# Kernel optimization log

Measured on AMD Instinct MI355X. Metric: run time of the kernel, lower is better.

Reference implementation:

```python
import jax, jax.numpy as jnp
import numpy as np

NUM_HEADS = 16

def setup_inputs() -> dict:
    key = jax.random.key(0)
    ks = jax.random.split(key, 7)
    B, S, D = 2, 2048, 1024
    X = jax.random.normal(ks[0], (B, S, D), dtype=jnp.float32)
    s = 1.0 / np.sqrt(D)
    Wq = jax.random.normal(ks[1], (D, D), dtype=jnp.float32) * s
    Wk = jax.random.normal(ks[2], (D, D), dtype=jnp.float32) * s
    Wv = jax.random.normal(ks[3], (D, D), dtype=jnp.float32) * s
    Wo = jax.random.normal(ks[4], (D, D), dtype=jnp.float32) * s
    bo = jnp.zeros((D,), dtype=jnp.float32)
    return {"X": X, "Wq": Wq, "Wk": Wk, "Wv": Wv, "Wo": Wo, "bo": bo}

def reference(X, Wq, Wk, Wv, Wo, bo):
    B, S, D = X.shape
    H = NUM_HEADS
    hd = D // H
    # project and split heads -> [B, H, S, hd]
    def split(t):
        return t.reshape(B, S, H, hd).transpose(0, 2, 1, 3)
    q = split(X @ Wq)
    k = split(X @ Wk)
    v = split(X @ Wv)
    scores = jnp.einsum('bhqd,bhkd->bhqk', q, k) / jnp.sqrt(jnp.float32(hd))
    causal = jnp.tril(jnp.ones((S, S), dtype=bool))
    scores = jnp.where(causal, scores, -jnp.inf)
    weights = jax.nn.softmax(scores, axis=-1)  # dropout p=0 -> identity
    ctx = jnp.einsum('bhqk,bhkd->bhqd', weights, v)
    ctx = ctx.transpose(0, 2, 1, 3).reshape(B, S, D)
    return ctx @ Wo + bo
```

## Files before the change

### kernel.cpp

```cpp
#include <hip/hip_runtime.h>


typedef __attribute__((ext_vector_type(8))) short short8;
typedef __attribute__((ext_vector_type(4))) float floatx4;

__device__ inline float bf2f(unsigned short u) {
  return __uint_as_float(((unsigned)u) << 16);
}
__device__ inline unsigned short f2bf(float f) {
  unsigned u = __float_as_uint(f);
  unsigned r = (u + 0x7fffu + ((u >> 16) & 1u)) >> 16;
  return (unsigned short)r;
}

__device__ __forceinline__ void gll16(const unsigned short* g, unsigned short* l) {
  __builtin_amdgcn_global_load_lds(
      (const __attribute__((address_space(1))) unsigned int*)(g),
      (__attribute__((address_space(3))) unsigned int*)(l),
      16, 0, 0);
}

constexpr int B_ = 2, S_ = 2048, D_ = 1024, H_ = 16, HD_ = 64;

__global__ __launch_bounds__(256) void convert_x(
    const float* __restrict__ x, unsigned short* __restrict__ xb)
{
  const size_t i = ((size_t)blockIdx.x * 256 + threadIdx.x) * 8;
  float4 a = *(const float4*)(x + i);
  float4 b = *(const float4*)(x + i + 4);
  short8 o;
  o[0] = (short)f2bf(a.x); o[1] = (short)f2bf(a.y);
  o[2] = (short)f2bf(a.z); o[3] = (short)f2bf(a.w);
  o[4] = (short)f2bf(b.x); o[5] = (short)f2bf(b.y);
  o[6] = (short)f2bf(b.z); o[7] = (short)f2bf(b.w);
  *(short8*)(xb + i) = o;
}

__global__ __launch_bounds__(256) void transpose_convert_w4(
    const float* __restrict__ w0, const float* __restrict__ w1,
    const float* __restrict__ w2, const float* __restrict__ w3,
    unsigned short* __restrict__ wt_base)
{
  const float* src;
  switch (blockIdx.z) {
    case 0: src = w0; break;
    case 1: src = w1; break;
    case 2: src = w2; break;
    default: src = w3; break;
  }
  unsigned short* dst = wt_base + (size_t)blockIdx.z * 1024 * 1024;
  __shared__ unsigned short t[32][33];
  const int bx = blockIdx.x * 32;
  const int by = blockIdx.y * 32;
  const int x = threadIdx.x;
  for (int yy = threadIdx.y; yy < 32; yy += 8)
    t[yy][x] = f2bf(src[(size_t)(by + yy) * 1024 + bx + x]);
  __syncthreads();
  for (int yy = threadIdx.y; yy < 32; yy += 8)
    dst[(size_t)(bx + yy) * 1024 + by + x] = t[x][yy];
}

__global__ __launch_bounds__(256) void transpose_v(
    const unsigned short* __restrict__ Vb, unsigned short* __restrict__ Vt)
{
  __shared__ unsigned short t[32][33];
  const int bh = blockIdx.z;
  const int b = bh >> 4, h = bh & 15;
  const int s0 = blockIdx.x * 32, d0 = blockIdx.y * 32;
  const int x = threadIdx.x;
  for (int yy = threadIdx.y; yy < 32; yy += 8)
    t[yy][x] = Vb[(size_t)(b * 2048 + s0 + yy) * 1024 + h * 64 + d0 + x];
  __syncthreads();
  for (int yy = threadIdx.y; yy < 32; yy += 8)
    Vt[((size_t)bh * 64 + d0 + yy) * 2048 + s0 + x] = t[x][yy];
}

struct GemmAcc { floatx4 a[4][4]; };

__device__ __forceinline__ void gemm256_core(
    const unsigned short* __restrict__ A,
    const unsigned short* __restrict__ Bt,
    int m0, int bn0, int K,
    unsigned short* sA, unsigned short* sB, GemmAcc& acc)
{
  const int tid = threadIdx.x, wave = tid >> 6, lane = tid & 63;
  const int g = lane >> 4, ml = lane & 15;
  const int wm = wave & 1, wn = wave >> 1;

  const unsigned short* ag0 = A + (size_t)(m0 + (tid >> 2)) * K + (tid & 3) * 8;
  const unsigned short* ag1 = ag0 + (size_t)64 * K;
  const unsigned short* bg0 = Bt + (size_t)(bn0 + (tid >> 2)) * K + (tid & 3) * 8;
  const unsigned short* bg1 = bg0 + (size_t)64 * K;
  unsigned short* sAw0 = sA + wave * 512;
  unsigned short* sAw1 = sA + 2048 + wave * 512;
  unsigned short* sBw0 = sB + wave * 512;
  unsigned short* sBw1 = sB + 2048 + wave * 512;

#pragma unroll
  for (int mt = 0; mt < 4; ++mt)
#pragma unroll
    for (int nt = 0; nt < 4; ++nt) acc.a[mt][nt] = (floatx4){0.f, 0.f, 0.f, 0.f};

  for (int k0 = 0; k0 < K; k0 += 32) {
    __syncthreads();
    gll16(ag0 + k0, sAw0);
    gll16(ag1 + k0, sAw1);
    gll16(bg0 + k0, sBw0);
    gll16(bg1 + k0, sBw1);
    __syncthreads();
    short8 af[4], bf[4];
#pragma unroll
    for (int mt = 0; mt < 4; ++mt)
      af[mt] = *(const short8*)(sA + (wm * 64 + mt * 16 + ml) * 32 + g * 8);
#pragma unroll
    for (int nt = 0; nt < 4; ++nt)
      bf[nt] = *(const short8*)(sB + (wn * 64 + nt * 16 + ml) * 32 + g * 8);
#pragma unroll
    for (int mt = 0; mt < 4; ++mt)
#pragma unroll
      for (int nt = 0; nt < 4; ++nt)
        acc.a[mt][nt] = __builtin_amdgcn_mfma_f32_16x16x32_bf16(
            af[mt], bf[nt], acc.a[mt][nt], 0, 0, 0);
  }
}

__global__ __launch_bounds__(256) void gemm256_qkv(
    const unsigned short* __restrict__ A,
    const unsigned short* __restrict__ Bt,
    unsigned short* __restrict__ Qo,
    unsigned short* __restrict__ Ko,
    unsigned short* __restrict__ Vo)
{
  __shared__ unsigned short sA[128 * 32];
  __shared__ unsigned short sB[128 * 32];
  const int m0 = blockIdx.y * 128;
  const int bn0 = blockIdx.x * 128;
  GemmAcc acc;
  gemm256_core(A, Bt, m0, bn0, 1024, sA, sB, acc);

  const int proj = blockIdx.x >> 3;
  unsigned short* out = (proj == 0) ? Qo : (proj == 1) ? Ko : Vo;
  const int col0 = (blockIdx.x & 7) * 128;
  const int tid = threadIdx.x, wave = tid >> 6, lane = tid & 63;
  const int g = lane >> 4, ml = lane & 15;
  const int wm = wave & 1, wn = wave >> 1;
#pragma unroll
  for (int mt = 0; mt < 4; ++mt) {
#pragma unroll
    for (int nt = 0; nt < 4; ++nt) {
      const int col = col0 + wn * 64 + nt * 16 + ml;
#pragma unroll
      for (int r = 0; r < 4; ++r) {
        const int row = m0 + wm * 64 + mt * 16 + g * 4 + r;
        out[(size_t)row * 1024 + col] = f2bf(acc.a[mt][nt][r]);
      }
    }
  }
}

__global__ __launch_bounds__(256) void gemm256_wo(
    const unsigned short* __restrict__ A,
    const unsigned short* __restrict__ Bt,
    const float* __restrict__ bias,
    float* __restrict__ C)
{
  __shared__ unsigned short sA[128 * 32];
  __shared__ unsigned short sB[128 * 32];
  const int m0 = blockIdx.y * 128;
  const int bn0 = blockIdx.x * 128;
  GemmAcc acc;
  gemm256_core(A, Bt, m0, bn0, 1024, sA, sB, acc);

  const int tid = threadIdx.x, wave = tid >> 6, lane = tid & 63;
  const int g = lane >> 4, ml = lane & 15;
  const int wm = wave & 1, wn = wave >> 1;
#pragma unroll
  for (int mt = 0; mt < 4; ++mt) {
#pragma unroll
    for (int nt = 0; nt < 4; ++nt) {
      const int col = bn0 + wn * 64 + nt * 16 + ml;
      const float badd = bias[col];
#pragma unroll
      for (int r = 0; r < 4; ++r) {
        const int row = m0 + wm * 64 + mt * 16 + g * 4 + r;
        C[(size_t)row * 1024 + col] = acc.a[mt][nt][r] + badd;
      }
    }
  }
}

constexpr int LDP = 72;

__device__ __forceinline__ void attn_tile(
    const short8* aq,
    const unsigned short* sK0, const unsigned short* sK1,
    const unsigned short* sV0, const unsigned short* sV1,
    unsigned short* pw, floatx4* acc, float* l,
    const bool diag, const int qrow0, const int kcol0,
    const int g, const int ml)
{
  floatx4 s[4];
#pragma unroll
  for (int nb = 0; nb < 4; ++nb) {
    s[nb] = (floatx4){0.f, 0.f, 0.f, 0.f};
    short8 bk0 = *(const short8*)(sK0 + (nb * 16 + ml) * 32 + g * 8);
    s[nb] = __builtin_amdgcn_mfma_f32_16x16x32_bf16(aq[0], bk0, s[nb], 0, 0, 0);
    short8 bk1 = *(const short8*)(sK1 + (nb * 16 + ml) * 32 + g * 8);
    s[nb] = __builtin_amdgcn_mfma_f32_16x16x32_bf16(aq[1], bk1, s[nb], 0, 0, 0);
  }
#pragma unroll
  for (int r = 0; r < 4; ++r) {
    const int qrow = qrow0 + g * 4 + r;
    float rowsum = 0.f;
#pragma unroll
    for (int nb = 0; nb < 4; ++nb) {
      float wv = __expf(fmaf(s[nb][r], 0.125f, -24.0f));
      if (diag && (kcol0 + nb * 16 + ml > qrow)) wv = 0.f;
      rowsum += wv;
      pw[(g * 4 + r) * LDP + nb * 16 + ml] = f2bf(wv);
    }
    l[r] += rowsum;
  }
#pragma unroll
  for (int st = 0; st < 2; ++st) {
    short8 ap = *(const short8*)(pw + ml * LDP + st * 32 + g * 8);
    const unsigned short* sv = st ? sV1 : sV0;
#pragma unroll
    for (int jd = 0; jd < 4; ++jd) {
      short8 bv = *(const short8*)(sv + (jd * 16 + ml) * 32 + g * 8);
      acc[jd] = __builtin_amdgcn_mfma_f32_16x16x32_bf16(ap, bv, acc[jd], 0, 0, 0);
    }
  }
}

__global__ __launch_bounds__(256) void attn_v2(
    const unsigned short* __restrict__ Q,
    const unsigned short* __restrict__ Kg,
    const unsigned short* __restrict__ Vt,
    unsigned short* __restrict__ CTX)
{
  __shared__ unsigned short sK0[64 * 32], sK1[64 * 32];
  __shared__ unsigned short sV0[64 * 32], sV1[64 * 32];
  __shared__ unsigned short sP[4 * 16 * LDP];

  const int bh = blockIdx.y;
  const int b = bh >> 4, h = bh & 15;
  const int p = blockIdx.x;
  const int qbA = p, qbB = 31 - p;
  const int qA0 = qbA * 64, qB0 = qbB * 64;
  const int tid = threadIdx.x, wave = tid >> 6, lane = tid & 63;
  const int g = lane >> 4, ml = lane & 15;

  const size_t headoff = (size_t)b * S_ * D_ + (size_t)h * HD_;
  const size_t vtoff   = (size_t)bh * HD_ * S_;

  short8 aqA[2], aqB[2];
  {
    const unsigned short* qp =
        Q + headoff + (size_t)(qA0 + wave * 16 + ml) * D_ + g * 8;
    aqA[0] = *(const short8*)qp;
    aqA[1] = *(const short8*)(qp + 32);
  }
  {
    const unsigned short* qp =
        Q + headoff + (size_t)(qB0 + wave * 16 + ml) * D_ + g * 8;
    aqB[0] = *(const short8*)qp;
    aqB[1] = *(const short8*)(qp + 32);
  }

  floatx4 accA[4], accB[4];
#pragma unroll
  for (int jd = 0; jd < 4; ++jd) {
    accA[jd] = (floatx4){0.f, 0.f, 0.f, 0.f};
    accB[jd] = (floatx4){0.f, 0.f, 0.f, 0.f};
  }
  float lA[4] = {0.f, 0.f, 0.f, 0.f};
  float lB[4] = {0.f, 0.f, 0.f, 0.f};

  const int srow = lane >> 2;
  const int schunk = (lane & 3) * 8;
  const unsigned short* kgb =
      Kg + headoff + (size_t)(wave * 16 + srow) * D_ + schunk;
  const unsigned short* vgb =
      Vt + vtoff + (size_t)(wave * 16 + srow) * S_ + schunk;
  unsigned short* sk0w = sK0 + wave * 16 * 32;
  unsigned short* sk1w = sK1 + wave * 16 * 32;
  unsigned short* sv0w = sV0 + wave * 16 * 32;
  unsigned short* sv1w = sV1 + wave * 16 * 32;
  unsigned short* pw = sP + wave * 16 * LDP;

  for (int kt = 0; kt <= qbB; ++kt) {
    __syncthreads();
    const size_t ko = (size_t)kt * 64 * D_;
    gll16(kgb + ko, sk0w);
    gll16(kgb + ko + 32, sk1w);
    gll16(vgb + kt * 64, sv0w);
    gll16(vgb + kt * 64 + 32, sv1w);
    __syncthreads();

    attn_tile(aqB, sK0, sK1, sV0, sV1, pw, accB, lB,
              kt == qbB, qB0 + wave * 16, kt * 64, g, ml);
    if (kt <= qbA)
      attn_tile(aqA, sK0, sK1, sV0, sV1, pw, accA, lA,
                kt == qbA, qA0 + wave * 16, kt * 64, g, ml);
  }

#pragma unroll
  for (int r = 0; r < 4; ++r) {
    float la = lA[r];
    la += __shfl_xor(la, 1); la += __shfl_xor(la, 2);
    la += __shfl_xor(la, 4); la += __shfl_xor(la, 8);
    lA[r] = 1.0f / la;
    float lb = lB[r];
    lb += __shfl_xor(lb, 1); lb += __shfl_xor(lb, 2);
    lb += __shfl_xor(lb, 4); lb += __shfl_xor(lb, 8);
    lB[r] = 1.0f / lb;
  }
#pragma unroll
  for (int r = 0; r < 4; ++r) {
    const int rowA = qA0 + wave * 16 + g * 4 + r;
    const int rowB = qB0 + wave * 16 + g * 4 + r;
#pragma unroll
    for (int jd = 0; jd < 4; ++jd) {
      CTX[headoff + (size_t)rowA * D_ + jd * 16 + ml] = f2bf(accA[jd][r] * lA[r]);
      CTX[headoff + (size_t)rowB * D_ + jd * 16 + ml] = f2bf(accB[jd][r] * lB[r]);
    }
  }
}

constexpr int LDK = 40;

__global__ __launch_bounds__(256) void gemm_f32_bf16(
    const float* __restrict__ A, const float* __restrict__ B,
    unsigned short* __restrict__ C, int M, int N, int K)
{
  __shared__ unsigned short sA[64 * LDK];
  __shared__ unsigned short sB[64 * LDK];
  const int tid = threadIdx.x, wave = tid >> 6, lane = tid & 63;
  const int n0 = blockIdx.x * 64, m0 = blockIdx.y * 64;
  const int a_row = tid >> 2, a_k = (tid & 3) * 8;
  const float* Ag = A + (size_t)(m0 + a_row) * K + a_k;
  unsigned short* sAw = sA + a_row * LDK + a_k;
  const int b_k = tid >> 3, b_n = (tid & 7) * 8;
  const float* Bg = B + (size_t)b_k * N + n0 + b_n;
  unsigned short* sBw = sB + b_n * LDK + b_k;
  const int q = lane >> 4, ml = lane & 15;
  const unsigned short* sAr = sA + (wave * 16 + ml) * LDK + q * 8;
  const unsigned short* sBr = sB + ml * LDK + q * 8;
  floatx4 acc[4];
#pragma unroll
  for (int j = 0; j < 4; ++j) acc[j] = (floatx4){0.f, 0.f, 0.f, 0.f};
  for (int k0 = 0; k0 < K; k0 += 32) {
    float4 av0 = *(const float4*)(Ag + k0);
    float4 av1 = *(const float4*)(Ag + k0 + 4);
    float4 bv0 = *(const float4*)(Bg + (size_t)k0 * N);
    float4 bv1 = *(const float4*)(Bg + (size_t)k0 * N + 4);
    short8 av;
    av[0] = (short)f2bf(av0.x); av[1] = (short)f2bf(av0.y);
    av[2] = (short)f2bf(av0.z); av[3] = (short)f2bf(av0.w);
    av[4] = (short)f2bf(av1.x); av[5] = (short)f2bf(av1.y);
    av[6] = (short)f2bf(av1.z); av[7] = (short)f2bf(av1.w);
    __syncthreads();
    *(short8*)sAw = av;
    sBw[0 * LDK] = f2bf(bv0.x); sBw[1 * LDK] = f2bf(bv0.y);
    sBw[2 * LDK] = f2bf(bv0.z); sBw[3 * LDK] = f2bf(bv0.w);
    sBw[4 * LDK] = f2bf(bv1.x); sBw[5 * LDK] = f2bf(bv1.y);
    sBw[6 * LDK] = f2bf(bv1.z); sBw[7 * LDK] = f2bf(bv1.w);
    __syncthreads();
    short8 af = *(const short8*)sAr;
#pragma unroll
    for (int j = 0; j < 4; ++j) {
      short8 bf = *(const short8*)(sBr + j * 16 * LDK);
      acc[j] = __builtin_amdgcn_mfma_f32_16x16x32_bf16(af, bf, acc[j], 0, 0, 0);
    }
  }
#pragma unroll
  for (int j = 0; j < 4; ++j) {
    const int col = n0 + j * 16 + ml;
#pragma unroll
    for (int r = 0; r < 4; ++r) {
      const int row = m0 + wave * 16 + q * 4 + r;
      C[(size_t)row * N + col] = f2bf(acc[j][r]);
    }
  }
}

__global__ __launch_bounds__(256) void gemm_bf16_f32(
    const unsigned short* __restrict__ A, const float* __restrict__ B,
    const float* __restrict__ bias, float* __restrict__ C, int M, int N, int K)
{
  __shared__ unsigned short sA[64 * LDK];
  __shared__ unsigned short sB[64 * LDK];
  const int tid = threadIdx.x, wave = tid >> 6, lane = tid & 63;
  const int n0 = blockIdx.x * 64, m0 = blockIdx.y * 64;
  const int a_row = tid >> 2, a_k = (tid & 3) * 8;
  const unsigned short* Ag = A + (size_t)(m0 + a_row) * K + a_k;
  unsigned short* sAw = sA + a_row * LDK + a_k;
  const int b_k = tid >> 3, b_n = (tid & 7) * 8;
  const float* Bg = B + (size_t)b_k * N + n0 + b_n;
  unsigned short* sBw = sB + b_n * LDK + b_k;
  const int q = lane >> 4, ml = lane & 15;
  const unsigned short* sAr = sA + (wave * 16 + ml) * LDK + q * 8;
  const unsigned short* sBr = sB + ml * LDK + q * 8;
  floatx4 acc[4];
#pragma unroll
  for (int j = 0; j < 4; ++j) acc[j] = (floatx4){0.f, 0.f, 0.f, 0.f};
  for (int k0 = 0; k0 < K; k0 += 32) {
    short8 av = *(const short8*)(Ag + k0);
    float4 bv0 = *(const float4*)(Bg + (size_t)k0 * N);
    float4 bv1 = *(const float4*)(Bg + (size_t)k0 * N + 4);
    __syncthreads();
    *(short8*)sAw = av;
    sBw[0 * LDK] = f2bf(bv0.x); sBw[1 * LDK] = f2bf(bv0.y);
    sBw[2 * LDK] = f2bf(bv0.z); sBw[3 * LDK] = f2bf(bv0.w);
    sBw[4 * LDK] = f2bf(bv1.x); sBw[5 * LDK] = f2bf(bv1.y);
    sBw[6 * LDK] = f2bf(bv1.z); sBw[7 * LDK] = f2bf(bv1.w);
    __syncthreads();
    short8 af = *(const short8*)sAr;
#pragma unroll
    for (int j = 0; j < 4; ++j) {
      short8 bf = *(const short8*)(sBr + j * 16 * LDK);
      acc[j] = __builtin_amdgcn_mfma_f32_16x16x32_bf16(af, bf, acc[j], 0, 0, 0);
    }
  }
#pragma unroll
  for (int j = 0; j < 4; ++j) {
    const int col = n0 + j * 16 + ml;
    const float badd = bias[col];
#pragma unroll
    for (int r = 0; r < 4; ++r) {
      const int row = m0 + wave * 16 + q * 4 + r;
      C[(size_t)row * N + col] = acc[j][r] + badd;
    }
  }
}

constexpr int LDT = HD_ + 8;

__global__ __launch_bounds__(256) void attn_mfma(
    const unsigned short* __restrict__ Q,
    const unsigned short* __restrict__ Kg,
    const unsigned short* __restrict__ V,
    unsigned short* __restrict__ CTX)
{
  __shared__ unsigned short sK[64 * LDT];
  __shared__ unsigned short sVt[64 * LDT];
  __shared__ unsigned short sP[4 * 16 * LDT];

  const int bh = blockIdx.y;
  const int b = bh >> 4, h = bh & 15;
  const int qb = (S_ / 64 - 1) - blockIdx.x;
  const int q0 = qb * 64;
  const int tid = threadIdx.x, wave = tid >> 6, lane = tid & 63;
  const int g = lane >> 4, ml = lane & 15;

  const size_t headoff = (size_t)b * S_ * D_ + (size_t)h * HD_;

  short8 a_q[2];
  {
    const unsigned short* qp =
        Q + headoff + (size_t)(q0 + wave * 16 + ml) * D_ + g * 8;
    a_q[0] = *(const short8*)(qp);
    a_q[1] = *(const short8*)(qp + 32);
  }

  floatx4 acc_o[4];
#pragma unroll
  for (int jd = 0; jd < 4; ++jd) acc_o[jd] = (floatx4){0.f, 0.f, 0.f, 0.f};
  float m_r[4], l_r[4];
#pragma unroll
  for (int r = 0; r < 4; ++r) { m_r[r] = -1e30f; l_r[r] = 0.f; }

  const int stg_key = tid >> 2;
  const int stg_d   = (tid & 3) * 16;
  const unsigned short* kbase = Kg + headoff;
  const unsigned short* vbase = V + headoff;

  for (int kt = 0; kt <= qb; ++kt) {
    __syncthreads();
    {
      const unsigned short* kp = kbase + (size_t)(kt * 64 + stg_key) * D_ + stg_d;
      const unsigned short* vp = vbase + (size_t)(kt * 64 + stg_key) * D_ + stg_d;
      short8 k0 = *(const short8*)kp;
      short8 k1 = *(const short8*)(kp + 8);
      short8 v0 = *(const short8*)vp;
      short8 v1 = *(const short8*)(vp + 8);
      *(short8*)(sK + stg_key * LDT + stg_d)     = k0;
      *(short8*)(sK + stg_key * LDT + stg_d + 8) = k1;
#pragma unroll
      for (int j = 0; j < 8; ++j) {
        sVt[(stg_d + j) * LDT + stg_key]     = (unsigned short)v0[j];
        sVt[(stg_d + 8 + j) * LDT + stg_key] = (unsigned short)v1[j];
      }
    }
    __syncthreads();

    floatx4 s[4];
#pragma unroll
    for (int nb = 0; nb < 4; ++nb) {
      s[nb] = (floatx4){0.f, 0.f, 0.f, 0.f};
#pragma unroll
      for (int st = 0; st < 2; ++st) {
        short8 bk = *(const short8*)(sK + (nb * 16 + ml) * LDT + st * 32 + g * 8);
        s[nb] = __builtin_amdgcn_mfma_f32_16x16x32_bf16(a_q[st], bk, s[nb], 0, 0, 0);
      }
    }

    if (kt == qb) {
#pragma unroll
      for (int nb = 0; nb < 4; ++nb) {
        const int kcol = kt * 64 + nb * 16 + ml;
#pragma unroll
        for (int r = 0; r < 4; ++r) {
          const int qrow = q0 + wave * 16 + g * 4 + r;
          float sv = s[nb][r] * 0.125f;
          s[nb][r] = (kcol <= qrow) ? sv : -1e30f;
        }
      }
    } else {
#pragma unroll
      for (int nb = 0; nb < 4; ++nb)
#pragma unroll
        for (int r = 0; r < 4; ++r) s[nb][r] *= 0.125f;
    }

    unsigned short* pw = sP + wave * 16 * LDT;
#pragma unroll
    for (int r = 0; r < 4; ++r) {
      float mx = fmaxf(fmaxf(s[0][r], s[1][r]), fmaxf(s[2][r], s[3][r]));
      mx = fmaxf(mx, __shfl_xor(mx, 1));
      mx = fmaxf(mx, __shfl_xor(mx, 2));
      mx = fmaxf(mx, __shfl_xor(mx, 4));
      mx = fmaxf(mx, __shfl_xor(mx, 8));
      const float m_new = fmaxf(m_r[r], mx);
      const float alpha = __expf(m_r[r] - m_new);
      m_r[r] = m_new;
      float rs = 0.f;
#pragma unroll
      for (int nb = 0; nb < 4; ++nb) {
        const float w = __expf(s[nb][r] - m_new);
        s[nb][r] = w;
        rs += w;
      }
      rs += __shfl_xor(rs, 1);
      rs += __shfl_xor(rs, 2);
      rs += __shfl_xor(rs, 4);
      rs += __shfl_xor(rs, 8);
      l_r[r] = l_r[r] * alpha + rs;
#pragma unroll
      for (int jd = 0; jd < 4; ++jd) acc_o[jd][r] *= alpha;
#pragma unroll
      for (int nb = 0; nb < 4; ++nb)
        pw[(g * 4 + r) * LDT + nb * 16 + ml] = f2bf(s[nb][r]);
    }

#pragma unroll
    for (int st = 0; st < 2; ++st) {
      short8 ap = *(const short8*)(pw + ml * LDT + st * 32 + g * 8);
#pragma unroll
      for (int jd = 0; jd < 4; ++jd) {
        short8 bv = *(const short8*)(sVt + (jd * 16 + ml) * LDT + st * 32 + g * 8);
        acc_o[jd] = __builtin_amdgcn_mfma_f32_16x16x32_bf16(ap, bv, acc_o[jd], 0, 0, 0);
      }
    }
  }

#pragma unroll
  for (int r = 0; r < 4; ++r) {
    const float inv = 1.0f / l_r[r];
    const int qrow = q0 + wave * 16 + g * 4 + r;
#pragma unroll
    for (int jd = 0; jd < 4; ++jd) {
      CTX[headoff + (size_t)qrow * D_ + jd * 16 + ml] = f2bf(acc_o[jd][r] * inv);
    }
  }
}

extern "C" void kernel_launch(void* const* d_in, const int* in_sizes, int n_in,
                              void* d_out, int out_size, void* d_ws, size_t ws_size,
                              hipStream_t stream)
{
  const float* X  = (const float*)d_in[0];
  const float* Wq = (const float*)d_in[1];
  const float* Wk = (const float*)d_in[2];
  const float* Wv = (const float*)d_in[3];
  const float* Wo = (const float*)d_in[4];
  const float* bo = (const float*)d_in[5];

  char* ws = (char*)d_ws;
  const size_t MB = 1024 * 1024;

  if (ws_size >= 32 * MB) {
    unsigned short* Qb  = (unsigned short*)(ws);
    unsigned short* Kb  = (unsigned short*)(ws + 8 * MB);
    unsigned short* Xb  = (unsigned short*)(ws + 16 * MB);
    unsigned short* WT  = (unsigned short*)(ws + 24 * MB);
    unsigned short* WoT = WT + (size_t)3 * 1024 * 1024;
    unsigned short* Vb  = (unsigned short*)d_out;
    unsigned short* Vt  = Xb;

    convert_x<<<2048, 256, 0, stream>>>(X, Xb);
    transpose_convert_w4<<<dim3(32, 32, 4), dim3(32, 8), 0, stream>>>(
        Wq, Wk, Wv, Wo, WT);
    gemm256_qkv<<<dim3(24, 32), 256, 0, stream>>>(Xb, WT, Qb, Kb, Vb);
    transpose_v<<<dim3(64, 2, 32), dim3(32, 8), 0, stream>>>(Vb, Vt);
    attn_v2<<<dim3(16, B_ * H_), 256, 0, stream>>>(Qb, Kb, Vt, Qb);
    gemm256_wo<<<dim3(8, 32), 256, 0, stream>>>(Qb, WoT, bo, (float*)d_out);
  } else {
    unsigned short* Qb = (unsigned short*)(ws);
    unsigned short* Kb = (unsigned short*)(ws + 8 * MB);
    unsigned short* Vb = (unsigned short*)d_out;

    gemm_f32_bf16<<<dim3(16, 64), 256, 0, stream>>>(X, Wq, Qb, 4096, 1024, 1024);
    gemm_f32_bf16<<<dim3(16, 64), 256, 0, stream>>>(X, Wk, Kb, 4096, 1024, 1024);
    gemm_f32_bf16<<<dim3(16, 64), 256, 0, stream>>>(X, Wv, Vb, 4096, 1024, 1024);
    attn_mfma<<<dim3(S_ / 64, B_ * H_), 256, 0, stream>>>(Qb, Kb, Vb, Qb);
    gemm_bf16_f32<<<dim3(16, 64), 256, 0, stream>>>(Qb, Wo, bo, (float*)d_out,
                                                    4096, 1024, 1024);
  }
}
```

Baseline: 203.7 us.

## Split attention into one q-block per workgroup and shrink Wo GEMM tile

Attention blocks no longer pair a short and a long causal q-block. Each block now handles a single q-block, the grid doubles to 32 blocks per head, and the longest blocks are scheduled first. The softmax uses exp2 with a folded scale and fixed offset, and the row sum is taken from the truncated bf16 value so it matches the stored weights. The output-projection GEMM drops from 128-row to 64-row tiles with its own simple loop, giving twice as many workgroups for better CU occupancy at the cost of less reuse of each loaded tile. The fallback path for a small workspace is removed.

```diff
diff --git a/kernel.cpp b/kernel.cpp
--- a/kernel.cpp
+++ b/kernel.cpp
@@ -4,9 +4,6 @@
 typedef __attribute__((ext_vector_type(8))) short short8;
 typedef __attribute__((ext_vector_type(4))) float floatx4;
 
-__device__ inline float bf2f(unsigned short u) {
-  return __uint_as_float(((unsigned)u) << 16);
-}
 __device__ inline unsigned short f2bf(float f) {
   unsigned u = __float_as_uint(f);
   unsigned r = (u + 0x7fffu + ((u >> 16) & 1u)) >> 16;
@@ -158,32 +155,66 @@
   }
 }
 
-__global__ __launch_bounds__(256) void gemm256_wo(
+__global__ __launch_bounds__(256) void gemm_wo64(
     const unsigned short* __restrict__ A,
     const unsigned short* __restrict__ Bt,
     const float* __restrict__ bias,
     float* __restrict__ C)
 {
-  __shared__ unsigned short sA[128 * 32];
+  __shared__ unsigned short sA[64 * 32];
   __shared__ unsigned short sB[128 * 32];
-  const int m0 = blockIdx.y * 128;
+  const int K = 1024;
+  const int m0 = blockIdx.y * 64;
   const int bn0 = blockIdx.x * 128;
-  GemmAcc acc;
-  gemm256_core(A, Bt, m0, bn0, 1024, sA, sB, acc);
-
   const int tid = threadIdx.x, wave = tid >> 6, lane = tid & 63;
   const int g = lane >> 4, ml = lane & 15;
   const int wm = wave & 1, wn = wave >> 1;
-#pragma unroll
-  for (int mt = 0; mt < 4; ++mt) {
+
+  const unsigned short* ag =
+      A + (size_t)(m0 + wave * 16 + (lane >> 2)) * K + (lane & 3) * 8;
+  const unsigned short* bg0 = Bt + (size_t)(bn0 + (tid >> 2)) * K + (tid & 3) * 8;
+  const unsigned short* bg1 = bg0 + (size_t)64 * K;
+  unsigned short* sAw  = sA + wave * 512;
+  unsigned short* sBw0 = sB + wave * 512;
+  unsigned short* sBw1 = sB + 2048 + wave * 512;
+
+  floatx4 acc[2][4];
+#pragma unroll
+  for (int mt = 0; mt < 2; ++mt)
+#pragma unroll
+    for (int nt = 0; nt < 4; ++nt) acc[mt][nt] = (floatx4){0.f, 0.f, 0.f, 0.f};
+
+  for (int k0 = 0; k0 < K; k0 += 32) {
+    __syncthreads();
+    gll16(ag + k0, sAw);
+    gll16(bg0 + k0, sBw0);
+    gll16(bg1 + k0, sBw1);
+    __syncthreads();
+    short8 af[2], bf[4];
+#pragma unroll
+    for (int mt = 0; mt < 2; ++mt)
+      af[mt] = *(const short8*)(sA + (wm * 32 + mt * 16 + ml) * 32 + g * 8);
+#pragma unroll
+    for (int nt = 0; nt < 4; ++nt)
+      bf[nt] = *(const short8*)(sB + (wn * 64 + nt * 16 + ml) * 32 + g * 8);
+#pragma unroll
+    for (int mt = 0; mt < 2; ++mt)
+#pragma unroll
+      for (int nt = 0; nt < 4; ++nt)
+        acc[mt][nt] = __builtin_amdgcn_mfma_f32_16x16x32_bf16(
+            af[mt], bf[nt], acc[mt][nt], 0, 0, 0);
+  }
+
+#pragma unroll
+  for (int mt = 0; mt < 2; ++mt) {
 #pragma unroll
     for (int nt = 0; nt < 4; ++nt) {
       const int col = bn0 + wn * 64 + nt * 16 + ml;
       const float badd = bias[col];
 #pragma unroll
       for (int r = 0; r < 4; ++r) {
-        const int row = m0 + wm * 64 + mt * 16 + g * 4 + r;
-        C[(size_t)row * 1024 + col] = acc.a[mt][nt][r] + badd;
+        const int row = m0 + wm * 32 + mt * 16 + g * 4 + r;
+        C[(size_t)row * 1024 + col] = acc[mt][nt][r] + badd;
       }
     }
   }
@@ -191,49 +222,7 @@
 
 constexpr int LDP = 72;
 
-__device__ __forceinline__ void attn_tile(
-    const short8* aq,
-    const unsigned short* sK0, const unsigned short* sK1,
-    const unsigned short* sV0, const unsigned short* sV1,
-    unsigned short* pw, floatx4* acc, float* l,
-    const bool diag, const int qrow0, const int kcol0,
-    const int g, const int ml)
-{
-  floatx4 s[4];
-#pragma unroll
-  for (int nb = 0; nb < 4; ++nb) {
-    s[nb] = (floatx4){0.f, 0.f, 0.f, 0.f};
-    short8 bk0 = *(const short8*)(sK0 + (nb * 16 + ml) * 32 + g * 8);
-    s[nb] = __builtin_amdgcn_mfma_f32_16x16x32_bf16(aq[0], bk0, s[nb], 0, 0, 0);
-    short8 bk1 = *(const short8*)(sK1 + (nb * 16 + ml) * 32 + g * 8);
-    s[nb] = __builtin_amdgcn_mfma_f32_16x16x32_bf16(aq[1], bk1, s[nb], 0, 0, 0);
-  }
-#pragma unroll
-  for (int r = 0; r < 4; ++r) {
-    const int qrow = qrow0 + g * 4 + r;
-    float rowsum = 0.f;
-#pragma unroll
-    for (int nb = 0; nb < 4; ++nb) {
-      float wv = __expf(fmaf(s[nb][r], 0.125f, -24.0f));
-      if (diag && (kcol0 + nb * 16 + ml > qrow)) wv = 0.f;
-      rowsum += wv;
-      pw[(g * 4 + r) * LDP + nb * 16 + ml] = f2bf(wv);
-    }
-    l[r] += rowsum;
-  }
-#pragma unroll
-  for (int st = 0; st < 2; ++st) {
-    short8 ap = *(const short8*)(pw + ml * LDP + st * 32 + g * 8);
-    const unsigned short* sv = st ? sV1 : sV0;
-#pragma unroll
-    for (int jd = 0; jd < 4; ++jd) {
-      short8 bv = *(const short8*)(sv + (jd * 16 + ml) * 32 + g * 8);
-      acc[jd] = __builtin_amdgcn_mfma_f32_16x16x32_bf16(ap, bv, acc[jd], 0, 0, 0);
-    }
-  }
-}
-
-__global__ __launch_bounds__(256) void attn_v2(
+__global__ __launch_bounds__(256) void attn_v3(
     const unsigned short* __restrict__ Q,
     const unsigned short* __restrict__ Kg,
     const unsigned short* __restrict__ Vt,
@@ -245,51 +234,41 @@
 
   const int bh = blockIdx.y;
   const int b = bh >> 4, h = bh & 15;
-  const int p = blockIdx.x;
-  const int qbA = p, qbB = 31 - p;
-  const int qA0 = qbA * 64, qB0 = qbB * 64;
+  const int qb = 31 - blockIdx.x;
+  const int q0 = qb * 64;
   const int tid = threadIdx.x, wave = tid >> 6, lane = tid & 63;
   const int g = lane >> 4, ml = lane & 15;
 
   const size_t headoff = (size_t)b * S_ * D_ + (size_t)h * HD_;
   const size_t vtoff   = (size_t)bh * HD_ * S_;
 
-  short8 aqA[2], aqB[2];
+  short8 aq[2];
   {
     const unsigned short* qp =
-        Q + headoff + (size_t)(qA0 + wave * 16 + ml) * D_ + g * 8;
-    aqA[0] = *(const short8*)qp;
-    aqA[1] = *(const short8*)(qp + 32);
-  }
-  {
-    const unsigned short* qp =
-        Q + headoff + (size_t)(qB0 + wave * 16 + ml) * D_ + g * 8;
-    aqB[0] = *(const short8*)qp;
-    aqB[1] = *(const short8*)(qp + 32);
-  }
-
-  floatx4 accA[4], accB[4];
-#pragma unroll
-  for (int jd = 0; jd < 4; ++jd) {
-    accA[jd] = (floatx4){0.f, 0.f, 0.f, 0.f};
-    accB[jd] = (floatx4){0.f, 0.f, 0.f, 0.f};
-  }
-  float lA[4] = {0.f, 0.f, 0.f, 0.f};
-  float lB[4] = {0.f, 0.f, 0.f, 0.f};
-
-  const int srow = lane >> 2;
-  const int schunk = (lane & 3) * 8;
+        Q + headoff + (size_t)(q0 + wave * 16 + ml) * D_ + g * 8;
+    aq[0] = *(const short8*)qp;
+    aq[1] = *(const short8*)(qp + 32);
+  }
+
+  floatx4 acc[4];
+#pragma unroll
+  for (int jd = 0; jd < 4; ++jd) acc[jd] = (floatx4){0.f, 0.f, 0.f, 0.f};
+  float l[4] = {0.f, 0.f, 0.f, 0.f};
+
   const unsigned short* kgb =
-      Kg + headoff + (size_t)(wave * 16 + srow) * D_ + schunk;
+      Kg + headoff + (size_t)(wave * 16 + (lane >> 2)) * D_ + (lane & 3) * 8;
   const unsigned short* vgb =
-      Vt + vtoff + (size_t)(wave * 16 + srow) * S_ + schunk;
-  unsigned short* sk0w = sK0 + wave * 16 * 32;
-  unsigned short* sk1w = sK1 + wave * 16 * 32;
-  unsigned short* sv0w = sV0 + wave * 16 * 32;
-  unsigned short* sv1w = sV1 + wave * 16 * 32;
+      Vt + vtoff + (size_t)(wave * 16 + (lane >> 2)) * S_ + (lane & 3) * 8;
+  unsigned short* sk0w = sK0 + wave * 512;
+  unsigned short* sk1w = sK1 + wave * 512;
+  unsigned short* sv0w = sV0 + wave * 512;
+  unsigned short* sv1w = sV1 + wave * 512;
   unsigned short* pw = sP + wave * 16 * LDP;
 
-  for (int kt = 0; kt <= qbB; ++kt) {
+  const float C1 = 0.18033688f;
+  const float C2 = -34.6246810f;
+
+  for (int kt = 0; kt <= qb; ++kt) {
     __syncthreads();
     const size_t ko = (size_t)kt * 64 * D_;
     gll16(kgb + ko, sk0w);
@@ -298,281 +277,54 @@
     gll16(vgb + kt * 64 + 32, sv1w);
     __syncthreads();
 
-    attn_tile(aqB, sK0, sK1, sV0, sV1, pw, accB, lB,
-              kt == qbB, qB0 + wave * 16, kt * 64, g, ml);
-    if (kt <= qbA)
-      attn_tile(aqA, sK0, sK1, sV0, sV1, pw, accA, lA,
-                kt == qbA, qA0 + wave * 16, kt * 64, g, ml);
-  }
-
-#pragma unroll
-  for (int r = 0; r < 4; ++r) {
-    float la = lA[r];
-    la += __shfl_xor(la, 1); la += __shfl_xor(la, 2);
-    la += __shfl_xor(la, 4); la += __shfl_xor(la, 8);
-    lA[r] = 1.0f / la;
-    float lb = lB[r];
-    lb += __shfl_xor(lb, 1); lb += __shfl_xor(lb, 2);
-    lb += __shfl_xor(lb, 4); lb += __shfl_xor(lb, 8);
-    lB[r] = 1.0f / lb;
-  }
-#pragma unroll
-  for (int r = 0; r < 4; ++r) {
-    const int rowA = qA0 + wave * 16 + g * 4 + r;
-    const int rowB = qB0 + wave * 16 + g * 4 + r;
-#pragma unroll
-    for (int jd = 0; jd < 4; ++jd) {
-      CTX[headoff + (size_t)rowA * D_ + jd * 16 + ml] = f2bf(accA[jd][r] * lA[r]);
-      CTX[headoff + (size_t)rowB * D_ + jd * 16 + ml] = f2bf(accB[jd][r] * lB[r]);
-    }
-  }
-}
-
-constexpr int LDK = 40;
-
-__global__ __launch_bounds__(256) void gemm_f32_bf16(
-    const float* __restrict__ A, const float* __restrict__ B,
-    unsigned short* __restrict__ C, int M, int N, int K)
-{
-  __shared__ unsigned short sA[64 * LDK];
-  __shared__ unsigned short sB[64 * LDK];
-  const int tid = threadIdx.x, wave = tid >> 6, lane = tid & 63;
-  const int n0 = blockIdx.x * 64, m0 = blockIdx.y * 64;
-  const int a_row = tid >> 2, a_k = (tid & 3) * 8;
-  const float* Ag = A + (size_t)(m0 + a_row) * K + a_k;
-  unsigned short* sAw = sA + a_row * LDK + a_k;
-  const int b_k = tid >> 3, b_n = (tid & 7) * 8;
-  const float* Bg = B + (size_t)b_k * N + n0 + b_n;
-  unsigned short* sBw = sB + b_n * LDK + b_k;
-  const int q = lane >> 4, ml = lane & 15;
-  const unsigned short* sAr = sA + (wave * 16 + ml) * LDK + q * 8;
-  const unsigned short* sBr = sB + ml * LDK + q * 8;
-  floatx4 acc[4];
-#pragma unroll
-  for (int j = 0; j < 4; ++j) acc[j] = (floatx4){0.f, 0.f, 0.f, 0.f};
-  for (int k0 = 0; k0 < K; k0 += 32) {
-    float4 av0 = *(const float4*)(Ag + k0);
-    float4 av1 = *(const float4*)(Ag + k0 + 4);
-    float4 bv0 = *(const float4*)(Bg + (size_t)k0 * N);
-    float4 bv1 = *(const float4*)(Bg + (size_t)k0 * N + 4);
-    short8 av;
-    av[0] = (short)f2bf(av0.x); av[1] = (short)f2bf(av0.y);
-    av[2] = (short)f2bf(av0.z); av[3] = (short)f2bf(av0.w);
-    av[4] = (short)f2bf(av1.x); av[5] = (short)f2bf(av1.y);
-    av[6] = (short)f2bf(av1.z); av[7] = (short)f2bf(av1.w);
-    __syncthreads();
-    *(short8*)sAw = av;
-    sBw[0 * LDK] = f2bf(bv0.x); sBw[1 * LDK] = f2bf(bv0.y);
-    sBw[2 * LDK] = f2bf(bv0.z); sBw[3 * LDK] = f2bf(bv0.w);
-    sBw[4 * LDK] = f2bf(bv1.x); sBw[5 * LDK] = f2bf(bv1.y);
-    sBw[6 * LDK] = f2bf(bv1.z); sBw[7 * LDK] = f2bf(bv1.w);
-    __syncthreads();
-    short8 af = *(const short8*)sAr;
-#pragma unroll
-    for (int j = 0; j < 4; ++j) {
-      short8 bf = *(const short8*)(sBr + j * 16 * LDK);
-      acc[j] = __builtin_amdgcn_mfma_f32_16x16x32_bf16(af, bf, acc[j], 0, 0, 0);
-    }
-  }
-#pragma unroll
-  for (int j = 0; j < 4; ++j) {
-    const int col = n0 + j * 16 + ml;
-#pragma unroll
-    for (int r = 0; r < 4; ++r) {
-      const int row = m0 + wave * 16 + q * 4 + r;
-      C[(size_t)row * N + col] = f2bf(acc[j][r]);
-    }
-  }
-}
-
-__global__ __launch_bounds__(256) void gemm_bf16_f32(
-    const unsigned short* __restrict__ A, const float* __restrict__ B,
-    const float* __restrict__ bias, float* __restrict__ C, int M, int N, int K)
-{
-  __shared__ unsigned short sA[64 * LDK];
-  __shared__ unsigned short sB[64 * LDK];
-  const int tid = threadIdx.x, wave = tid >> 6, lane = tid & 63;
-  const int n0 = blockIdx.x * 64, m0 = blockIdx.y * 64;
-  const int a_row = tid >> 2, a_k = (tid & 3) * 8;
-  const unsigned short* Ag = A + (size_t)(m0 + a_row) * K + a_k;
-  unsigned short* sAw = sA + a_row * LDK + a_k;
-  const int b_k = tid >> 3, b_n = (tid & 7) * 8;
-  const float* Bg = B + (size_t)b_k * N + n0 + b_n;
-  unsigned short* sBw = sB + b_n * LDK + b_k;
-  const int q = lane >> 4, ml = lane & 15;
-  const unsigned short* sAr = sA + (wave * 16 + ml) * LDK + q * 8;
-  const unsigned short* sBr = sB + ml * LDK + q * 8;
-  floatx4 acc[4];
-#pragma unroll
-  for (int j = 0; j < 4; ++j) acc[j] = (floatx4){0.f, 0.f, 0.f, 0.f};
-  for (int k0 = 0; k0 < K; k0 += 32) {
-    short8 av = *(const short8*)(Ag + k0);
-    float4 bv0 = *(const float4*)(Bg + (size_t)k0 * N);
-    float4 bv1 = *(const float4*)(Bg + (size_t)k0 * N + 4);
-    __syncthreads();
-    *(short8*)sAw = av;
-    sBw[0 * LDK] = f2bf(bv0.x); sBw[1 * LDK] = f2bf(bv0.y);
-    sBw[2 * LDK] = f2bf(bv0.z); sBw[3 * LDK] = f2bf(bv0.w);
-    sBw[4 * LDK] = f2bf(bv1.x); sBw[5 * LDK] = f2bf(bv1.y);
-    sBw[6 * LDK] = f2bf(bv1.z); sBw[7 * LDK] = f2bf(bv1.w);
-    __syncthreads();
-    short8 af = *(const short8*)sAr;
-#pragma unroll
-    for (int j = 0; j < 4; ++j) {
-      short8 bf = *(const short8*)(sBr + j * 16 * LDK);
-      acc[j] = __builtin_amdgcn_mfma_f32_16x16x32_bf16(af, bf, acc[j], 0, 0, 0);
-    }
-  }
-#pragma unroll
-  for (int j = 0; j < 4; ++j) {
-    const int col = n0 + j * 16 + ml;
-    const float badd = bias[col];
-#pragma unroll
-    for (int r = 0; r < 4; ++r) {
-      const int row = m0 + wave * 16 + q * 4 + r;
-      C[(size_t)row * N + col] = acc[j][r] + badd;
-    }
-  }
-}
-
-constexpr int LDT = HD_ + 8;
-
-__global__ __launch_bounds__(256) void attn_mfma(
-    const unsigned short* __restrict__ Q,
-    const unsigned short* __restrict__ Kg,
-    const unsigned short* __restrict__ V,
-    unsigned short* __restrict__ CTX)
-{
-  __shared__ unsigned short sK[64 * LDT];
-  __shared__ unsigned short sVt[64 * LDT];
-  __shared__ unsigned short sP[4 * 16 * LDT];
-
-  const int bh = blockIdx.y;
-  const int b = bh >> 4, h = bh & 15;
-  const int qb = (S_ / 64 - 1) - blockIdx.x;
-  const int q0 = qb * 64;
-  const int tid = threadIdx.x, wave = tid >> 6, lane = tid & 63;
-  const int g = lane >> 4, ml = lane & 15;
-
-  const size_t headoff = (size_t)b * S_ * D_ + (size_t)h * HD_;
-
-  short8 a_q[2];
-  {
-    const unsigned short* qp =
-        Q + headoff + (size_t)(q0 + wave * 16 + ml) * D_ + g * 8;
-    a_q[0] = *(const short8*)(qp);
-    a_q[1] = *(const short8*)(qp + 32);
-  }
-
-  floatx4 acc_o[4];
-#pragma unroll
-  for (int jd = 0; jd < 4; ++jd) acc_o[jd] = (floatx4){0.f, 0.f, 0.f, 0.f};
-  float m_r[4], l_r[4];
-#pragma unroll
-  for (int r = 0; r < 4; ++r) { m_r[r] = -1e30f; l_r[r] = 0.f; }
-
-  const int stg_key = tid >> 2;
-  const int stg_d   = (tid & 3) * 16;
-  const unsigned short* kbase = Kg + headoff;
-  const unsigned short* vbase = V + headoff;
-
-  for (int kt = 0; kt <= qb; ++kt) {
-    __syncthreads();
-    {
-      const unsigned short* kp = kbase + (size_t)(kt * 64 + stg_key) * D_ + stg_d;
-      const unsigned short* vp = vbase + (size_t)(kt * 64 + stg_key) * D_ + stg_d;
-      short8 k0 = *(const short8*)kp;
-      short8 k1 = *(const short8*)(kp + 8);
-      short8 v0 = *(const short8*)vp;
-      short8 v1 = *(const short8*)(vp + 8);
-      *(short8*)(sK + stg_key * LDT + stg_d)     = k0;
-      *(short8*)(sK + stg_key * LDT + stg_d + 8) = k1;
-#pragma unroll
-      for (int j = 0; j < 8; ++j) {
-        sVt[(stg_d + j) * LDT + stg_key]     = (unsigned short)v0[j];
-        sVt[(stg_d + 8 + j) * LDT + stg_key] = (unsigned short)v1[j];
-      }
-    }
-    __syncthreads();
-
     floatx4 s[4];
 #pragma unroll
     for (int nb = 0; nb < 4; ++nb) {
       s[nb] = (floatx4){0.f, 0.f, 0.f, 0.f};
-#pragma unroll
-      for (int st = 0; st < 2; ++st) {
-        short8 bk = *(const short8*)(sK + (nb * 16 + ml) * LDT + st * 32 + g * 8);
-        s[nb] = __builtin_amdgcn_mfma_f32_16x16x32_bf16(a_q[st], bk, s[nb], 0, 0, 0);
+      short8 bk0 = *(const short8*)(sK0 + (nb * 16 + ml) * 32 + g * 8);
+      s[nb] = __builtin_amdgcn_mfma_f32_16x16x32_bf16(aq[0], bk0, s[nb], 0, 0, 0);
+      short8 bk1 = *(const short8*)(sK1 + (nb * 16 + ml) * 32 + g * 8);
+      s[nb] = __builtin_amdgcn_mfma_f32_16x16x32_bf16(aq[1], bk1, s[nb], 0, 0, 0);
+    }
+
+    const bool diag = (kt == qb);
+#pragma unroll
+    for (int r = 0; r < 4; ++r) {
+      const int qrow = q0 + wave * 16 + g * 4 + r;
+      float rowsum = 0.f;
+#pragma unroll
+      for (int nb = 0; nb < 4; ++nb) {
+        float e = exp2f(fmaf(s[nb][r], C1, C2));
+        if (diag && (kt * 64 + nb * 16 + ml > qrow)) e = 0.f;
+        const unsigned bits = __float_as_uint(e);
+        pw[(g * 4 + r) * LDP + nb * 16 + ml] = (unsigned short)(bits >> 16);
+        rowsum += __uint_as_float(bits & 0xffff0000u);
       }
-    }
-
-    if (kt == qb) {
-#pragma unroll
-      for (int nb = 0; nb < 4; ++nb) {
-        const int kcol = kt * 64 + nb * 16 + ml;
-#pragma unroll
-        for (int r = 0; r < 4; ++r) {
-          const int qrow = q0 + wave * 16 + g * 4 + r;
-          float sv = s[nb][r] * 0.125f;
-          s[nb][r] = (kcol <= qrow) ? sv : -1e30f;
-        }
+      l[r] += rowsum;
+    }
+
+#pragma unroll
+    for (int st = 0; st < 2; ++st) {
+      short8 ap = *(const short8*)(pw + ml * LDP + st * 32 + g * 8);
+      const unsigned short* sv = st ? sV1 : sV0;
+#pragma unroll
+      for (int jd = 0; jd < 4; ++jd) {
+        short8 bv = *(const short8*)(sv + (jd * 16 + ml) * 32 + g * 8);
+        acc[jd] = __builtin_amdgcn_mfma_f32_16x16x32_bf16(ap, bv, acc[jd], 0, 0, 0);
       }
-    } else {
-#pragma unroll
-      for (int nb = 0; nb < 4; ++nb)
-#pragma unroll
-        for (int r = 0; r < 4; ++r) s[nb][r] *= 0.125f;
-    }
-
-    unsigned short* pw = sP + wave * 16 * LDT;
-#pragma unroll
-    for (int r = 0; r < 4; ++r) {
-      float mx = fmaxf(fmaxf(s[0][r], s[1][r]), fmaxf(s[2][r], s[3][r]));
-      mx = fmaxf(mx, __shfl_xor(mx, 1));
-      mx = fmaxf(mx, __shfl_xor(mx, 2));
-      mx = fmaxf(mx, __shfl_xor(mx, 4));
-      mx = fmaxf(mx, __shfl_xor(mx, 8));
-      const float m_new = fmaxf(m_r[r], mx);
-      const float alpha = __expf(m_r[r] - m_new);
-      m_r[r] = m_new;
-      float rs = 0.f;
-#pragma unroll
-      for (int nb = 0; nb < 4; ++nb) {
-        const float w = __expf(s[nb][r] - m_new);
-        s[nb][r] = w;
-        rs += w;
-      }
-      rs += __shfl_xor(rs, 1);
-      rs += __shfl_xor(rs, 2);
-      rs += __shfl_xor(rs, 4);
-      rs += __shfl_xor(rs, 8);
-      l_r[r] = l_r[r] * alpha + rs;
-#pragma unroll
-      for (int jd = 0; jd < 4; ++jd) acc_o[jd][r] *= alpha;
-#pragma unroll
-      for (int nb = 0; nb < 4; ++nb)
-        pw[(g * 4 + r) * LDT + nb * 16 + ml] = f2bf(s[nb][r]);
-    }
-
-#pragma unroll
-    for (int st = 0; st < 2; ++st) {
-      short8 ap = *(const short8*)(pw + ml * LDT + st * 32 + g * 8);
-#pragma unroll
-      for (int jd = 0; jd < 4; ++jd) {
-        short8 bv = *(const short8*)(sVt + (jd * 16 + ml) * LDT + st * 32 + g * 8);
-        acc_o[jd] = __builtin_amdgcn_mfma_f32_16x16x32_bf16(ap, bv, acc_o[jd], 0, 0, 0);
-      }
     }
   }
 
 #pragma unroll
   for (int r = 0; r < 4; ++r) {
-    const float inv = 1.0f / l_r[r];
-    const int qrow = q0 + wave * 16 + g * 4 + r;
-#pragma unroll
-    for (int jd = 0; jd < 4; ++jd) {
-      CTX[headoff + (size_t)qrow * D_ + jd * 16 + ml] = f2bf(acc_o[jd][r] * inv);
-    }
+    float lv = l[r];
+    lv += __shfl_xor(lv, 1); lv += __shfl_xor(lv, 2);
+    lv += __shfl_xor(lv, 4); lv += __shfl_xor(lv, 8);
+    const float inv = 1.0f / lv;
+    const int row = q0 + wave * 16 + g * 4 + r;
+#pragma unroll
+    for (int jd = 0; jd < 4; ++jd)
+      CTX[headoff + (size_t)row * D_ + jd * 16 + ml] = f2bf(acc[jd][r] * inv);
   }
 }
 
@@ -590,32 +342,19 @@
   char* ws = (char*)d_ws;
   const size_t MB = 1024 * 1024;
 
-  if (ws_size >= 32 * MB) {
-    unsigned short* Qb  = (unsigned short*)(ws);
-    unsigned short* Kb  = (unsigned short*)(ws + 8 * MB);
-    unsigned short* Xb  = (unsigned short*)(ws + 16 * MB);
-    unsigned short* WT  = (unsigned short*)(ws + 24 * MB);
-    unsigned short* WoT = WT + (size_t)3 * 1024 * 1024;
-    unsigned short* Vb  = (unsigned short*)d_out;
-    unsigned short* Vt  = Xb;
-
-    convert_x<<<2048, 256, 0, stream>>>(X, Xb);
-    transpose_convert_w4<<<dim3(32, 32, 4), dim3(32, 8), 0, stream>>>(
-        Wq, Wk, Wv, Wo, WT);
-    gemm256_qkv<<<dim3(24, 32), 256, 0, stream>>>(Xb, WT, Qb, Kb, Vb);
-    transpose_v<<<dim3(64, 2, 32), dim3(32, 8), 0, stream>>>(Vb, Vt);
-    attn_v2<<<dim3(16, B_ * H_), 256, 0, stream>>>(Qb, Kb, Vt, Qb);
-    gemm256_wo<<<dim3(8, 32), 256, 0, stream>>>(Qb, WoT, bo, (float*)d_out);
-  } else {
-    unsigned short* Qb = (unsigned short*)(ws);
-    unsigned short* Kb = (unsigned short*)(ws + 8 * MB);
-    unsigned short* Vb = (unsigned short*)d_out;
-
-    gemm_f32_bf16<<<dim3(16, 64), 256, 0, stream>>>(X, Wq, Qb, 4096, 1024, 1024);
-    gemm_f32_bf16<<<dim3(16, 64), 256, 0, stream>>>(X, Wk, Kb, 4096, 1024, 1024);
-    gemm_f32_bf16<<<dim3(16, 64), 256, 0, stream>>>(X, Wv, Vb, 4096, 1024, 1024);
-    attn_mfma<<<dim3(S_ / 64, B_ * H_), 256, 0, stream>>>(Qb, Kb, Vb, Qb);
-    gemm_bf16_f32<<<dim3(16, 64), 256, 0, stream>>>(Qb, Wo, bo, (float*)d_out,
-                                                    4096, 1024, 1024);
-  }
-}
+  unsigned short* Qb  = (unsigned short*)(ws);
+  unsigned short* Kb  = (unsigned short*)(ws + 8 * MB);
+  unsigned short* Xb  = (unsigned short*)(ws + 16 * MB);
+  unsigned short* WT  = (unsigned short*)(ws + 24 * MB);
+  unsigned short* WoT = WT + (size_t)3 * 1024 * 1024;
+  unsigned short* Vb  = (unsigned short*)d_out;
+  unsigned short* Vt  = Xb;
+
+  convert_x<<<2048, 256, 0, stream>>>(X, Xb);
+  transpose_convert_w4<<<dim3(32, 32, 4), dim3(32, 8), 0, stream>>>(
+      Wq, Wk, Wv, Wo, WT);
+  gemm256_qkv<<<dim3(24, 32), 256, 0, stream>>>(Xb, WT, Qb, Kb, Vb);
+  transpose_v<<<dim3(64, 2, 32), dim3(32, 8), 0, stream>>>(Vb, Vt);
+  attn_v3<<<dim3(32, B_ * H_), 256, 0, stream>>>(Qb, Kb, Vt, Qb);
+  gemm_wo64<<<dim3(8, 64), 256, 0, stream>>>(Qb, WoT, bo, (float*)d_out);
+}
```

Measured after the change: 222.2 us. 1.09x slower.
